# Performance work log

Measured on AMD Instinct MI355X. Metric: run time of the kernel, lower is better.

Reference implementation:

```python
import jax, jax.numpy as jnp
import numpy as np
import math

D_MODEL = 2048
NUM_HEADS = 16
D_K = D_MODEL // NUM_HEADS  # 128
SEQ_LEN = 2048
THETA = 10000.0
BATCH = 2


def setup_inputs() -> dict:
    key = jax.random.key(0)
    ks = jax.random.split(key, 5)
    std = (2.0 / (D_MODEL + D_MODEL)) ** 0.5
    return {
        "x": jax.random.normal(ks[0], (BATCH, SEQ_LEN, D_MODEL), dtype=jnp.float32),
        "Wq": jax.random.normal(ks[1], (D_MODEL, D_MODEL), dtype=jnp.float32) * std,
        "Wk": jax.random.normal(ks[2], (D_MODEL, D_MODEL), dtype=jnp.float32) * std,
        "Wv": jax.random.normal(ks[3], (D_MODEL, D_MODEL), dtype=jnp.float32) * std,
        "Wo": jax.random.normal(ks[4], (D_MODEL, D_MODEL), dtype=jnp.float32) * std,
    }


def _rope(t):
    # t: [B, H, S, d_k]; apply rotary embedding on interleaved even/odd pairs
    S = t.shape[-2]
    dk = t.shape[-1]
    inv_freq = jnp.exp(-math.log(THETA) * jnp.arange(0, dk, 2, dtype=jnp.float32) / dk)  # [dk/2]
    pos = jnp.arange(S, dtype=jnp.float32)
    freqs = pos[:, None] * inv_freq[None, :]  # [S, dk/2]
    cos = jnp.cos(freqs)
    sin = jnp.sin(freqs)
    t1 = t[..., ::2]   # [B, H, S, dk/2]
    t2 = t[..., 1::2]
    rot = jnp.stack([t1 * cos - t2 * sin, t1 * sin + t2 * cos], axis=-1)  # [B,H,S,dk/2,2]
    return rot.reshape(t.shape)


def reference(x, Wq, Wk, Wv, Wo):
    B, S, D = x.shape
    H, dk = NUM_HEADS, D // NUM_HEADS

    def split_heads(t):
        return t.reshape(B, S, H, dk).transpose(0, 2, 1, 3)  # [B,H,S,dk]

    q = split_heads(x @ Wq.T)
    k = split_heads(x @ Wk.T)
    v = split_heads(x @ Wv.T)

    q = _rope(q)
    k = _rope(k)

    scores = jnp.einsum("bhqd,bhkd->bhqk", q, k) / math.sqrt(dk)  # [B,H,S,S]
    causal = jnp.tril(jnp.ones((S, S), dtype=bool))
    scores = jnp.where(causal[None, None], scores, -jnp.inf)
    attn = jax.nn.softmax(scores, axis=-1)
    ctx = jnp.einsum("bhqk,bhkd->bhqd", attn, v)  # [B,H,S,dk]
    ctx = ctx.transpose(0, 2, 1, 3).reshape(B, S, D)
    return ctx @ Wo.T
```

## Files before the change

### kernel.cpp

```cpp
#include <hip/hip_runtime.h>
#include <stdint.h>
#include <type_traits>

#define S_LEN 2048
#define DM 2048
#define NH 16
#define DKH 128
#define NB 2
#define NROWS (NB * S_LEN)

typedef unsigned short u16;
typedef __attribute__((ext_vector_type(8))) __bf16 bf16x8;
typedef __attribute__((ext_vector_type(4))) float f32x4;

__device__ __forceinline__ float bf2f(u16 u) {
  union { unsigned u; float f; } v; v.u = ((unsigned)u) << 16; return v.f;
}
__device__ __forceinline__ u16 f2bf(float f) {
  union { float f; unsigned u; } v; v.f = f;
  unsigned r = v.u + 0x7FFFu + ((v.u >> 16) & 1u);
  return (u16)(r >> 16);
}

__device__ __forceinline__ void async_copy16(void* lds, const void* g) {
  __builtin_amdgcn_global_load_lds(
      (const __attribute__((address_space(1))) unsigned int*)g,
      (__attribute__((address_space(3))) unsigned int*)lds, 16, 0, 0);
}

__global__ void cast_all_kernel(const float* __restrict__ x, const float* __restrict__ wq,
                                const float* __restrict__ wk, const float* __restrict__ wv,
                                const float* __restrict__ wo, u16* __restrict__ xb,
                                u16* __restrict__ wqkv, u16* __restrict__ wob) {
  const int XN4 = NROWS * DM / 4;
  const int WN4 = DM * DM / 4;
  int total = XN4 + 4 * WN4;
  int stride = gridDim.x * blockDim.x;
  for (int i = blockIdx.x * blockDim.x + threadIdx.x; i < total; i += stride) {
    const float* s;
    u16* d;
    int j;
    if (i < XN4) {
      s = x; d = xb; j = i;
    } else {
      int k = i - XN4;
      int w = k >> 20;
      j = k & 0xFFFFF;
      if (w == 0) { s = wq; d = wqkv; }
      else if (w == 1) { s = wk; d = wqkv + (size_t)DM * DM; }
      else if (w == 2) { s = wv; d = wqkv + (size_t)2 * DM * DM; }
      else { s = wo; d = wob; }
    }
    float4 v = ((const float4*)s)[j];
    unsigned r0 = (unsigned)f2bf(v.x) | ((unsigned)f2bf(v.y) << 16);
    unsigned r1 = (unsigned)f2bf(v.z) | ((unsigned)f2bf(v.w) << 16);
    ((uint2*)d)[j] = make_uint2(r0, r1);
  }
}

__global__ void rope_table_kernel(float2* __restrict__ ctab) {
  int idx = blockIdx.x * blockDim.x + threadIdx.x;
  if (idx >= S_LEN * 64) return;
  int s = idx >> 6, i = idx & 63;
  float inv = expf(-9.210340371976184f * (float)i * (1.0f / 64.0f));
  float fr = (float)s * inv;
  ctab[idx] = make_float2(cosf(fr), sinf(fr));
}

template <int NSEG, int EPI>
__global__ __launch_bounds__(512, 1) void gemm256_kernel(const u16* __restrict__ A,
                                                         const u16* __restrict__ B,
                                                         void* __restrict__ C0,
                                                         void* __restrict__ C1,
                                                         void* __restrict__ C2,
                                                         const float2* __restrict__ ctab,
                                                         int M, int N, int Kd) {
  constexpr int BN = 64 * NSEG;
  constexpr int BSZ = BN * 128;
  constexpr int LDS_AE = 0, LDS_AO = 32768, LDS_BE = 65536, LDS_BO = 65536 + BSZ;

  extern __shared__ char smem[];
  u16* lds = (u16*)smem;

  int tid = threadIdx.x;
  int lane = tid & 63, wave = tid >> 6;
  int lr = lane & 15, lg = lane >> 4;
  int wm = wave >> 2, wn = wave & 3;

  int gx = gridDim.x, nwg = gx * gridDim.y;
  int bid = blockIdx.y * gx + blockIdx.x;
  int cpx = nwg >> 3;
  int swz = (bid & 7) * cpx + (bid >> 3);
  int tm = (swz / gx) * 256, tn = (swz % gx) * BN;

  int srow_in = lane >> 3;
  int scolb = ((lane & 7) * 16) ^ ((lane >> 3) << 4);

  const u16* Arows = A + (size_t)tm * Kd;
  const u16* Brows = B + (size_t)tn * Kd;

  auto stageA = [&](int aBase, int h, int kt) {
#pragma unroll
    for (int l = 0; l < 2; l++) {
      int ch = h * 16 + l * 8 + wave;
      async_copy16(lds + ((aBase + ch * 1024) >> 1),
                   Arows + (size_t)(ch * 8 + srow_in) * Kd + kt * 64 + (scolb >> 1));
    }
  };
  auto stageB = [&](int bBase, int s, int kt) {
    int ch = s * 8 + wave;
    async_copy16(lds + ((bBase + ch * 1024) >> 1),
                 Brows + (size_t)(ch * 8 + srow_in) * Kd + kt * 64 + (scolb >> 1));
  };

  int acolb[2];
#pragma unroll
  for (int ks = 0; ks < 2; ks++) acolb[ks] = (ks * 64 + lg * 16) ^ ((lr & 7) << 4);
  int aBaseW = wm * 128 * 128;
  int brow_b = (wn * 16 * NSEG + lr) * 128;

  f32x4 zero4 = {0.f, 0.f, 0.f, 0.f};
  f32x4 acc[8][NSEG];
#pragma unroll
  for (int i = 0; i < 8; i++)
#pragma unroll
    for (int j = 0; j < NSEG; j++) acc[i][j] = zero4;

  bf16x8 bpre[NSEG][2];
  bf16x8 af[2][2];

  auto loadB = [&](int bBase) {
#pragma unroll
    for (int nf = 0; nf < NSEG; nf++)
#pragma unroll
      for (int ks = 0; ks < 2; ks++)
        bpre[nf][ks] = *(const bf16x8*)&lds[(bBase + brow_b + nf * 2048 + acolb[ks]) >> 1];
  };
  auto readA = [&](int aBase, int q) {
#pragma unroll
    for (int dm = 0; dm < 2; dm++)
#pragma unroll
      for (int ks = 0; ks < 2; ks++)
        af[dm][ks] = *(const bf16x8*)&lds[(aBase + aBaseW + (2 * q + dm) * 2048 + lr * 128 +
                                           acolb[ks]) >> 1];
  };
  auto mfmaC = [&](auto qc) {
    constexpr int Q = decltype(qc)::value;
    __builtin_amdgcn_s_setprio(1);
#pragma unroll
    for (int dm = 0; dm < 2; dm++)
#pragma unroll
      for (int nf = 0; nf < NSEG; nf++)
#pragma unroll
        for (int ks = 0; ks < 2; ks++)
          acc[2 * Q + dm][nf] = __builtin_amdgcn_mfma_f32_16x16x32_bf16(
              af[dm][ks], bpre[nf][ks], acc[2 * Q + dm][nf], 0, 0, 0);
    __builtin_amdgcn_s_setprio(0);
  };
  auto bar_pre = [&]() {
    __builtin_amdgcn_s_barrier();
    asm volatile("s_waitcnt lgkmcnt(0)" ::: "memory");
    __builtin_amdgcn_sched_barrier(0);
  };
  auto vm_wait = [&]() {
    if constexpr (NSEG == 3) asm volatile("s_waitcnt vmcnt(3)" ::: "memory");
    else asm volatile("s_waitcnt vmcnt(2)" ::: "memory");
  };

  int nk = Kd >> 6;
  int nIter = nk >> 1;

  stageA(LDS_AE, 0, 0);
  stageA(LDS_AE, 1, 0);
#pragma unroll
  for (int s = 0; s < NSEG; s++) stageB(LDS_BE, s, 0);
#pragma unroll
  for (int s = 0; s < NSEG; s++) stageB(LDS_BO, s, 1);
  vm_wait();
  __builtin_amdgcn_s_barrier();

  for (int i = 0; i < nIter; i++) {
    int tO = 2 * i + 1;
    int tE2 = 2 * i + 2; if (tE2 > nk - 1) tE2 = nk - 1;
    int tO2 = 2 * i + 3; if (tO2 > nk - 1) tO2 = nk - 1;

    loadB(LDS_BE); readA(LDS_AE, 0);
    stageA(LDS_AO, 0, tO);
    asm volatile("s_waitcnt lgkmcnt(8)" ::: "memory");
    bar_pre();
    mfmaC(std::integral_constant<int, 0>{});
    __builtin_amdgcn_s_barrier();
    readA(LDS_AE, 1);
    stageA(LDS_AO, 1, tO);
    bar_pre();
    mfmaC(std::integral_constant<int, 1>{});
    __builtin_amdgcn_s_barrier();
    readA(LDS_AE, 2);
    stageB(LDS_BE, 0, tE2);
    if constexpr (NSEG == 3) stageB(LDS_BE, 1, tE2);
    bar_pre();
    mfmaC(std::integral_constant<int, 2>{});
    __builtin_amdgcn_s_barrier();
    readA(LDS_AE, 3);
    stageB(LDS_BE, NSEG - 1, tE2);
    vm_wait();
    bar_pre();
    mfmaC(std::integral_constant<int, 3>{});
    __builtin_amdgcn_s_barrier();
    loadB(LDS_BO); readA(LDS_AO, 0);
    stageA(LDS_AE, 0, tE2);
    asm volatile("s_waitcnt lgkmcnt(8)" ::: "memory");
    bar_pre();
    mfmaC(std::integral_constant<int, 0>{});
    __builtin_amdgcn_s_barrier();
    readA(LDS_AO, 1);
    stageA(LDS_AE, 1, tE2);
    bar_pre();
    mfmaC(std::integral_constant<int, 1>{});
    __builtin_amdgcn_s_barrier();
    readA(LDS_AO, 2);
    stageB(LDS_BO, 0, tO2);
    if constexpr (NSEG == 3) stageB(LDS_BO, 1, tO2);
    bar_pre();
    mfmaC(std::integral_constant<int, 2>{});
    __builtin_amdgcn_s_barrier();
    readA(LDS_AO, 3);
    stageB(LDS_BO, NSEG - 1, tO2);
    vm_wait();
    bar_pre();
    mfmaC(std::integral_constant<int, 3>{});
    __builtin_amdgcn_s_barrier();
  }

  asm volatile("s_waitcnt vmcnt(0)" ::: "memory");

#pragma unroll
  for (int mf = 0; mf < 8; mf++) {
    int row = tm + wm * 128 + mf * 16 + lg * 4;
#pragma unroll
    for (int nf = 0; nf < NSEG; nf++) {
      int col = tn + wn * 16 * NSEG + nf * 16 + lr;
      if constexpr (EPI == 0) {
        float* O = (float*)C0;
#pragma unroll
        for (int r = 0; r < 4; r++) O[(size_t)(row + r) * N + col] = acc[mf][nf][r];
      } else {
        int mat = col >> 11, lc = col & 2047;
        if (mat < 2) {
          u16* O = (mat == 0) ? (u16*)C0 : (u16*)C1;
          int d = lc & 127;
          bool odd = (d & 1) != 0;
          const float2* ct = ctab + (d >> 1);
#pragma unroll
          for (int r = 0; r < 4; r++) {
            float a = acc[mf][nf][r];
            float p = __shfl_xor(a, 1);
            int sIdx = (row + r) & (S_LEN - 1);
            float2 cs = ct[sIdx * 64];
            float o = odd ? (p * cs.y + a * cs.x) : (a * cs.x - p * cs.y);
            O[(size_t)(row + r) * 2048 + lc] = f2bf(o);
          }
        } else {
          u16* O = (u16*)C2;
          int h = lc >> 7, d = lc & 127;
          int bb = row >> 11, s0 = row & 2047;
          unsigned w0 = (unsigned)f2bf(acc[mf][nf][0]) | ((unsigned)f2bf(acc[mf][nf][1]) << 16);
          unsigned w1 = (unsigned)f2bf(acc[mf][nf][2]) | ((unsigned)f2bf(acc[mf][nf][3]) << 16);
          *(uint2*)(O + ((size_t)((bb * 16 + h) * 128 + d) * 2048 + s0)) = make_uint2(w0, w1);
        }
      }
    }
  }
}

__device__ __forceinline__ int kidx(int row, int colb) {
  return ((row << 8) + (colb ^ ((row & 7) << 4))) >> 1;
}
__device__ __forceinline__ int vidx(int row, int colb) {
  return ((row << 7) + (colb ^ ((row & 7) << 4))) >> 1;
}

__global__ __launch_bounds__(256, 2) void attn_kernel(const u16* __restrict__ Q,
                                                      const u16* __restrict__ K,
                                                      const u16* __restrict__ Vt,
                                                      u16* __restrict__ ctx) {
  __shared__ u16 Kl[2][64 * 128];
  __shared__ u16 Vl[2][128 * 64];

  int tid = threadIdx.x;
  int lane = tid & 63, wave = tid >> 6;
  int lr = lane & 15, lg = lane >> 4;
  int bh = blockIdx.x;
  int b = bh >> 4, h = bh & 15;
  int qt = (gridDim.y - 1) - blockIdx.y;
  int q0 = qt * 128;
  int q0w = q0 + wave * 32;

  bf16x8 qf[2][4];
#pragma unroll
  for (int mf = 0; mf < 2; mf++) {
    const u16* qbase = Q + (size_t)(b * S_LEN + q0w + mf * 16 + lr) * DM + h * DKH;
#pragma unroll
    for (int ks = 0; ks < 4; ks++) qf[mf][ks] = *(const bf16x8*)(qbase + ks * 32 + lg * 8);
  }

  f32x4 zero4 = {0.f, 0.f, 0.f, 0.f};
  f32x4 acc[2][8];
#pragma unroll
  for (int mf = 0; mf < 2; mf++)
#pragma unroll
    for (int f = 0; f < 8; f++) acc[mf][f] = zero4;
  float m_r[2], l_r[2];
#pragma unroll
  for (int mf = 0; mf < 2; mf++) { m_r[mf] = -3.0e38f; l_r[mf] = 0.f; }

  const float SL2E = 1.4426950408889634f * 0.08838834764831845f;
  const float RTHR = 64.0f;

  const u16* Kbh = K + (size_t)b * S_LEN * DM + h * DKH;
  const u16* Vbh = Vt + (size_t)(b * NH + h) * DKH * S_LEN;

  auto stage = [&](int buf, int kv0s) {
#pragma unroll
    for (int c = 0; c < 4; c++) {
      int ch = wave * 4 + c;
      int krow = ch * 4 + (lane >> 4);
      int kphi = (krow & 0x23) | ((krow & 0x10) >> 2) | ((krow & 0x0C) << 1);
      int kcb = ((((lane & 15) << 4) ^ ((krow & 7) << 4)) >> 1);
      async_copy16(&Kl[buf][ch * 512], Kbh + (size_t)(kv0s + kphi) * DM + kcb);
      int vrow = ch * 8 + (lane >> 3);
      int vcb = ((((lane & 7) << 4) ^ ((vrow & 7) << 4)) >> 1);
      async_copy16(&Vl[buf][ch * 512], Vbh + (size_t)vrow * S_LEN + kv0s + vcb);
    }
  };

  int ntiles = 2 * qt + 2;
  stage(0, 0);
  __syncthreads();
  int cur = 0;

  for (int t = 0; t < ntiles; t++) {
    int kv0 = t * 64;
    if (t + 1 < ntiles) stage(cur ^ 1, (t + 1) * 64);

    if (kv0 <= q0w + 31) {
      bool need_mask = (kv0 + 63 > q0w);

      f32x4 sf[4][2];
#pragma unroll
      for (int kf = 0; kf < 4; kf++)
#pragma unroll
        for (int mf = 0; mf < 2; mf++) sf[kf][mf] = zero4;
      __builtin_amdgcn_s_setprio(1);
#pragma unroll
      for (int ks = 0; ks < 4; ks++)
#pragma unroll
        for (int kf = 0; kf < 4; kf++) {
          bf16x8 kfrag = *(const bf16x8*)&Kl[cur][kidx(kf * 16 + lr, ks * 64 + lg * 16)];
          sf[kf][0] = __builtin_amdgcn_mfma_f32_16x16x32_bf16(kfrag, qf[0][ks], sf[kf][0], 0, 0, 0);
          sf[kf][1] = __builtin_amdgcn_mfma_f32_16x16x32_bf16(kfrag, qf[1][ks], sf[kf][1], 0, 0, 0);
        }
      __builtin_amdgcn_s_setprio(0);

      float sv[2][4][4];
      float mx[2];
#pragma unroll
      for (int mf = 0; mf < 2; mf++) {
        int qg = q0w + mf * 16 + lr;
        mx[mf] = -3.0e38f;
#pragma unroll
        for (int kf = 0; kf < 4; kf++) {
          int kvb = kv0 + (kf >> 1) * 32 + (kf & 1) * 4 + lg * 8;
#pragma unroll
          for (int r = 0; r < 4; r++) {
            float x = sf[kf][mf][r];
            if (need_mask) x = (kvb + r <= qg) ? x : -3.0e38f;
            sv[mf][kf][r] = x;
            mx[mf] = fmaxf(mx[mf], x);
          }
        }
        mx[mf] = fmaxf(mx[mf], __shfl_xor(mx[mf], 16));
        mx[mf] = fmaxf(mx[mf], __shfl_xor(mx[mf], 32));
      }

      bool need = (mx[0] > m_r[0] + RTHR) | (mx[1] > m_r[1] + RTHR);
      if (__any(need)) {
        float scs[2];
#pragma unroll
        for (int mf = 0; mf < 2; mf++) {
          float mnew = fmaxf(m_r[mf], mx[mf]);
          scs[mf] = __builtin_amdgcn_exp2f((m_r[mf] - mnew) * SL2E);
          m_r[mf] = mnew;
          l_r[mf] *= scs[mf];
        }
#pragma unroll
        for (int mf = 0; mf < 2; mf++) {
#pragma unroll
          for (int r = 0; r < 4; r++) {
            float sa = __shfl(scs[mf], (lane & 0x30) | (lg * 4 + r));
#pragma unroll
            for (int f = 0; f < 8; f++) acc[mf][f][r] *= sa;
          }
        }
      }

      bf16x8 pf[2][2];
#pragma unroll
      for (int mf = 0; mf < 2; mf++) {
        float rs = 0.f;
#pragma unroll
        for (int kf = 0; kf < 4; kf++)
#pragma unroll
          for (int r = 0; r < 4; r++) {
            float p = __builtin_amdgcn_exp2f((sv[mf][kf][r] - m_r[mf]) * SL2E);
            sv[mf][kf][r] = p;
            rs += p;
          }
        rs += __shfl_xor(rs, 16);
        rs += __shfl_xor(rs, 32);
        l_r[mf] += rs;
#pragma unroll
        for (int ks2 = 0; ks2 < 2; ks2++) {
          bf16x8 t2;
#pragma unroll
          for (int r = 0; r < 4; r++) {
            t2[r] = (__bf16)sv[mf][2 * ks2][r];
            t2[4 + r] = (__bf16)sv[mf][2 * ks2 + 1][r];
          }
          pf[mf][ks2] = t2;
        }
      }

      __builtin_amdgcn_s_setprio(1);
#pragma unroll
      for (int ks2 = 0; ks2 < 2; ks2++)
#pragma unroll
        for (int f = 0; f < 8; f++) {
          bf16x8 vf = *(const bf16x8*)&Vl[cur][vidx(f * 16 + lr, ks2 * 64 + lg * 16)];
          acc[0][f] = __builtin_amdgcn_mfma_f32_16x16x32_bf16(pf[0][ks2], vf, acc[0][f], 0, 0, 0);
          acc[1][f] = __builtin_amdgcn_mfma_f32_16x16x32_bf16(pf[1][ks2], vf, acc[1][f], 0, 0, 0);
        }
      __builtin_amdgcn_s_setprio(0);
    }
    __syncthreads();
    cur ^= 1;
  }

#pragma unroll
  for (int mf = 0; mf < 2; mf++) {
    float invl = 1.0f / l_r[mf];
#pragma unroll
    for (int r = 0; r < 4; r++) {
      float ia = __shfl(invl, (lane & 0x30) | (lg * 4 + r));
      int rowg = b * S_LEN + q0w + mf * 16 + lg * 4 + r;
#pragma unroll
      for (int f = 0; f < 8; f++) {
        int colg = h * DKH + f * 16 + lr;
        ctx[(size_t)rowg * DM + colg] = f2bf(acc[mf][f][r] * ia);
      }
    }
  }
}

extern "C" void kernel_launch(void* const* d_in, const int* in_sizes, int n_in,
                              void* d_out, int out_size, void* d_ws, size_t ws_size,
                              hipStream_t stream) {
  const float* x = (const float*)d_in[0];
  const float* Wq = (const float*)d_in[1];
  const float* Wk = (const float*)d_in[2];
  const float* Wv = (const float*)d_in[3];
  const float* Wo = (const float*)d_in[4];
  float* out = (float*)d_out;

  char* ws = (char*)d_ws;
  size_t off = 0;
  auto alloc = [&](size_t bytes) -> char* {
    char* p = ws + off;
    off += (bytes + 255) & ~(size_t)255;
    return p;
  };
  u16* xb = (u16*)alloc((size_t)NROWS * DM * 2);
  u16* wqkv = (u16*)alloc((size_t)3 * DM * DM * 2);
  u16* wob = (u16*)alloc((size_t)DM * DM * 2);
  u16* Qb = (u16*)alloc((size_t)NROWS * DM * 2);
  u16* Kb = (u16*)alloc((size_t)NROWS * DM * 2);
  u16* Vtb = (u16*)alloc((size_t)NROWS * DM * 2);
  float2* ctab = (float2*)alloc((size_t)S_LEN * 64 * 8);
  u16* ctx = xb;

  hipFuncSetAttribute((const void*)gemm256_kernel<3, 2>,
                      hipFuncAttributeMaxDynamicSharedMemorySize, 65536 + 2 * 192 * 128);
  hipFuncSetAttribute((const void*)gemm256_kernel<2, 0>,
                      hipFuncAttributeMaxDynamicSharedMemorySize, 65536 + 2 * 128 * 128);

  cast_all_kernel<<<2048, 256, 0, stream>>>(x, Wq, Wk, Wv, Wo, xb, wqkv, wob);
  rope_table_kernel<<<(S_LEN * 64 + 255) / 256, 256, 0, stream>>>(ctab);

  gemm256_kernel<3, 2><<<dim3(3 * DM / 192, NROWS / 256), 512, 65536 + 2 * 192 * 128, stream>>>(
      xb, wqkv, Qb, Kb, Vtb, ctab, NROWS, 3 * DM, DM);

  attn_kernel<<<dim3(NB * NH, S_LEN / 128), 256, 0, stream>>>(Qb, Kb, Vtb, ctx);

  gemm256_kernel<2, 0><<<dim3(DM / 128, NROWS / 256), 512, 65536 + 2 * 128 * 128, stream>>>(
      ctx, wob, out, nullptr, nullptr, nullptr, NROWS, DM, DM);
}
```

Before: 251.8 us.

## Replace two-stage unrolled GEMM pipeline with triple-buffered A and fixed 128-wide tiles

Rewrites the GEMM main loop from an unrolled even/odd double-buffer scheme into a per-k-tile loop. A goes through three rotating LDS buffers and B through two toggled buffers, with prefetch distance two. The QKV projection drops its 192-wide N tile for a 128-wide one, which adds workgroups and shrinks per-workgroup reuse. LDS use rises to 128 KiB, and prefetching deeper is meant to hide global-load latency behind MFMA work.

```diff
diff --git a/kernel.cpp b/kernel.cpp
--- a/kernel.cpp
+++ b/kernel.cpp
@@ -67,18 +67,20 @@
   ctab[idx] = make_float2(cosf(fr), sinf(fr));
 }
 
-template <int NSEG, int EPI>
-__global__ __launch_bounds__(512, 1) void gemm256_kernel(const u16* __restrict__ A,
+#define A_BUF0 0
+#define A_BUF1 32768
+#define A_BUF2 65536
+#define B_BUF0 98304
+#define B_TOGGLE 16384
+
+template <int EPI>
+__global__ __launch_bounds__(512, 1) void gemm4ph_kernel(const u16* __restrict__ A,
                                                          const u16* __restrict__ B,
                                                          void* __restrict__ C0,
                                                          void* __restrict__ C1,
                                                          void* __restrict__ C2,
                                                          const float2* __restrict__ ctab,
                                                          int M, int N, int Kd) {
-  constexpr int BN = 64 * NSEG;
-  constexpr int BSZ = BN * 128;
-  constexpr int LDS_AE = 0, LDS_AO = 32768, LDS_BE = 65536, LDS_BO = 65536 + BSZ;
-
   extern __shared__ char smem[];
   u16* lds = (u16*)smem;
 
@@ -91,7 +93,7 @@
   int bid = blockIdx.y * gx + blockIdx.x;
   int cpx = nwg >> 3;
   int swz = (bid & 7) * cpx + (bid >> 3);
-  int tm = (swz / gx) * 256, tn = (swz % gx) * BN;
+  int tm = (swz / gx) * 256, tn = (swz % gx) * 128;
 
   int srow_in = lane >> 3;
   int scolb = ((lane & 7) * 16) ^ ((lane >> 3) << 4);
@@ -116,22 +118,22 @@
   int acolb[2];
 #pragma unroll
   for (int ks = 0; ks < 2; ks++) acolb[ks] = (ks * 64 + lg * 16) ^ ((lr & 7) << 4);
-  int aBaseW = wm * 128 * 128;
-  int brow_b = (wn * 16 * NSEG + lr) * 128;
+  int aBaseW = wm * 16384;
+  int brow_b = (wn * 32 + lr) * 128;
 
   f32x4 zero4 = {0.f, 0.f, 0.f, 0.f};
-  f32x4 acc[8][NSEG];
+  f32x4 acc[8][2];
 #pragma unroll
   for (int i = 0; i < 8; i++)
 #pragma unroll
-    for (int j = 0; j < NSEG; j++) acc[i][j] = zero4;
-
-  bf16x8 bpre[NSEG][2];
+    for (int j = 0; j < 2; j++) acc[i][j] = zero4;
+
+  bf16x8 bpre[2][2];
   bf16x8 af[2][2];
 
   auto loadB = [&](int bBase) {
 #pragma unroll
-    for (int nf = 0; nf < NSEG; nf++)
+    for (int nf = 0; nf < 2; nf++)
 #pragma unroll
       for (int ks = 0; ks < 2; ks++)
         bpre[nf][ks] = *(const bf16x8*)&lds[(bBase + brow_b + nf * 2048 + acolb[ks]) >> 1];
@@ -150,7 +152,7 @@
 #pragma unroll
     for (int dm = 0; dm < 2; dm++)
 #pragma unroll
-      for (int nf = 0; nf < NSEG; nf++)
+      for (int nf = 0; nf < 2; nf++)
 #pragma unroll
         for (int ks = 0; ks < 2; ks++)
           acc[2 * Q + dm][nf] = __builtin_amdgcn_mfma_f32_16x16x32_bf16(
@@ -162,74 +164,48 @@
     asm volatile("s_waitcnt lgkmcnt(0)" ::: "memory");
     __builtin_amdgcn_sched_barrier(0);
   };
-  auto vm_wait = [&]() {
-    if constexpr (NSEG == 3) asm volatile("s_waitcnt vmcnt(3)" ::: "memory");
-    else asm volatile("s_waitcnt vmcnt(2)" ::: "memory");
-  };
 
   int nk = Kd >> 6;
-  int nIter = nk >> 1;
-
-  stageA(LDS_AE, 0, 0);
-  stageA(LDS_AE, 1, 0);
-#pragma unroll
-  for (int s = 0; s < NSEG; s++) stageB(LDS_BE, s, 0);
-#pragma unroll
-  for (int s = 0; s < NSEG; s++) stageB(LDS_BO, s, 1);
-  vm_wait();
+
+  int aCur = A_BUF0, aNext = A_BUF1, aN2 = A_BUF2;
+  int bCur = B_BUF0;
+
+  stageA(A_BUF0, 0, 0);
+  stageA(A_BUF0, 1, 0);
+  stageB(B_BUF0, 0, 0);
+  stageB(B_BUF0, 1, 0);
+  stageA(A_BUF1, 0, 1);
+  stageA(A_BUF1, 1, 1);
+  stageB(B_BUF0 ^ B_TOGGLE, 0, 1);
+  stageB(B_BUF0 ^ B_TOGGLE, 1, 1);
+  asm volatile("s_waitcnt vmcnt(6)" ::: "memory");
   __builtin_amdgcn_s_barrier();
 
-  for (int i = 0; i < nIter; i++) {
-    int tO = 2 * i + 1;
-    int tE2 = 2 * i + 2; if (tE2 > nk - 1) tE2 = nk - 1;
-    int tO2 = 2 * i + 3; if (tO2 > nk - 1) tO2 = nk - 1;
-
-    loadB(LDS_BE); readA(LDS_AE, 0);
-    stageA(LDS_AO, 0, tO);
-    asm volatile("s_waitcnt lgkmcnt(8)" ::: "memory");
+  for (int t = 0; t < nk; t++) {
+    int kt2 = t + 2; if (kt2 > nk - 1) kt2 = nk - 1;
+    loadB(bCur); readA(aCur, 0);
+    stageA(aN2, 0, kt2);
     bar_pre();
     mfmaC(std::integral_constant<int, 0>{});
     __builtin_amdgcn_s_barrier();
-    readA(LDS_AE, 1);
-    stageA(LDS_AO, 1, tO);
+    readA(aCur, 1);
+    stageA(aN2, 1, kt2);
     bar_pre();
     mfmaC(std::integral_constant<int, 1>{});
     __builtin_amdgcn_s_barrier();
-    readA(LDS_AE, 2);
-    stageB(LDS_BE, 0, tE2);
-    if constexpr (NSEG == 3) stageB(LDS_BE, 1, tE2);
+    readA(aCur, 2);
+    stageB(bCur, 0, kt2);
     bar_pre();
     mfmaC(std::integral_constant<int, 2>{});
     __builtin_amdgcn_s_barrier();
-    readA(LDS_AE, 3);
-    stageB(LDS_BE, NSEG - 1, tE2);
-    vm_wait();
+    readA(aCur, 3);
+    stageB(bCur, 1, kt2);
+    asm volatile("s_waitcnt vmcnt(6)" ::: "memory");
     bar_pre();
     mfmaC(std::integral_constant<int, 3>{});
     __builtin_amdgcn_s_barrier();
-    loadB(LDS_BO); readA(LDS_AO, 0);
-    stageA(LDS_AE, 0, tE2);
-    asm volatile("s_waitcnt lgkmcnt(8)" ::: "memory");
-    bar_pre();
-    mfmaC(std::integral_constant<int, 0>{});
-    __builtin_amdgcn_s_barrier();
-    readA(LDS_AO, 1);
-    stageA(LDS_AE, 1, tE2);
-    bar_pre();
-    mfmaC(std::integral_constant<int, 1>{});
-    __builtin_amdgcn_s_barrier();
-    readA(LDS_AO, 2);
-    stageB(LDS_BO, 0, tO2);
-    if constexpr (NSEG == 3) stageB(LDS_BO, 1, tO2);
-    bar_pre();
-    mfmaC(std::integral_constant<int, 2>{});
-    __builtin_amdgcn_s_barrier();
-    readA(LDS_AO, 3);
-    stageB(LDS_BO, NSEG - 1, tO2);
-    vm_wait();
-    bar_pre();
-    mfmaC(std::integral_constant<int, 3>{});
-    __builtin_amdgcn_s_barrier();
+    int tmp = aCur; aCur = aNext; aNext = aN2; aN2 = tmp;
+    bCur ^= B_TOGGLE;
   }
 
   asm volatile("s_waitcnt vmcnt(0)" ::: "memory");
@@ -238,8 +214,8 @@
   for (int mf = 0; mf < 8; mf++) {
     int row = tm + wm * 128 + mf * 16 + lg * 4;
 #pragma unroll
-    for (int nf = 0; nf < NSEG; nf++) {
-      int col = tn + wn * 16 * NSEG + nf * 16 + lr;
+    for (int nf = 0; nf < 2; nf++) {
+      int col = tn + wn * 32 + nf * 16 + lr;
       if constexpr (EPI == 0) {
         float* O = (float*)C0;
 #pragma unroll
@@ -488,19 +464,19 @@
   float2* ctab = (float2*)alloc((size_t)S_LEN * 64 * 8);
   u16* ctx = xb;
 
-  hipFuncSetAttribute((const void*)gemm256_kernel<3, 2>,
-                      hipFuncAttributeMaxDynamicSharedMemorySize, 65536 + 2 * 192 * 128);
-  hipFuncSetAttribute((const void*)gemm256_kernel<2, 0>,
-                      hipFuncAttributeMaxDynamicSharedMemorySize, 65536 + 2 * 128 * 128);
+  hipFuncSetAttribute((const void*)gemm4ph_kernel<2>,
+                      hipFuncAttributeMaxDynamicSharedMemorySize, 131072);
+  hipFuncSetAttribute((const void*)gemm4ph_kernel<0>,
+                      hipFuncAttributeMaxDynamicSharedMemorySize, 131072);
 
   cast_all_kernel<<<2048, 256, 0, stream>>>(x, Wq, Wk, Wv, Wo, xb, wqkv, wob);
   rope_table_kernel<<<(S_LEN * 64 + 255) / 256, 256, 0, stream>>>(ctab);
 
-  gemm256_kernel<3, 2><<<dim3(3 * DM / 192, NROWS / 256), 512, 65536 + 2 * 192 * 128, stream>>>(
+  gemm4ph_kernel<2><<<dim3(3 * DM / 128, NROWS / 256), 512, 131072, stream>>>(
       xb, wqkv, Qb, Kb, Vtb, ctab, NROWS, 3 * DM, DM);
 
   attn_kernel<<<dim3(NB * NH, S_LEN / 128), 256, 0, stream>>>(Qb, Kb, Vtb, ctx);
 
-  gemm256_kernel<2, 0><<<dim3(DM / 128, NROWS / 256), 512, 65536 + 2 * 128 * 128, stream>>>(
+  gemm4ph_kernel<0><<<dim3(DM / 128, NROWS / 256), 512, 131072, stream>>>(
       ctx, wob, out, nullptr, nullptr, nullptr, NROWS, DM, DM);
 }
```

Result: slower. 277.4 us (+10.1%).

## Pair short and long causal query tiles per attention block for load balance

Applied to the files above, without the earlier changes.

The attention kernel now runs 512-thread blocks, each owning two 128-row query tiles, p and 15-p, so every block does a similar amount of causal work. Each wave takes 16 rows from each tile, and a templated tile-compute lambda runs both halves while the short tile is still active, then only the long one. K/V staging is split across 8 waves and shared by both tiles, which halves the grid and removes the tail imbalance of the causal triangle. The cost is one block per CU under the new launch bounds, and more waves idle on the mask-only or single-half path.

```diff
diff --git a/kernel.cpp b/kernel.cpp
--- a/kernel.cpp
+++ b/kernel.cpp
@@ -254,10 +254,10 @@
 #pragma unroll
           for (int r = 0; r < 4; r++) {
             float a = acc[mf][nf][r];
-            float p = __shfl_xor(a, 1);
+            float pp = __shfl_xor(a, 1);
             int sIdx = (row + r) & (S_LEN - 1);
             float2 cs = ct[sIdx * 64];
-            float o = odd ? (p * cs.y + a * cs.x) : (a * cs.x - p * cs.y);
+            float o = odd ? (pp * cs.y + a * cs.x) : (a * cs.x - pp * cs.y);
             O[(size_t)(row + r) * 2048 + lc] = f2bf(o);
           }
         } else {
@@ -280,7 +280,7 @@
   return ((row << 7) + (colb ^ ((row & 7) << 4))) >> 1;
 }
 
-__global__ __launch_bounds__(256, 2) void attn_kernel(const u16* __restrict__ Q,
+__global__ __launch_bounds__(512, 1) void attn_kernel(const u16* __restrict__ Q,
                                                       const u16* __restrict__ K,
                                                       const u16* __restrict__ Vt,
                                                       u16* __restrict__ ctx) {
@@ -292,14 +292,15 @@
   int lr = lane & 15, lg = lane >> 4;
   int bh = blockIdx.x;
   int b = bh >> 4, h = bh & 15;
-  int qt = (gridDim.y - 1) - blockIdx.y;
-  int q0 = qt * 128;
-  int q0w = q0 + wave * 32;
+  int p = blockIdx.y;
+  int q0s = p * 128 + wave * 16;
+  int q0b = (15 - p) * 128 + wave * 16;
 
   bf16x8 qf[2][4];
 #pragma unroll
   for (int mf = 0; mf < 2; mf++) {
-    const u16* qbase = Q + (size_t)(b * S_LEN + q0w + mf * 16 + lr) * DM + h * DKH;
+    int base = mf ? q0b : q0s;
+    const u16* qbase = Q + (size_t)(b * S_LEN + base + lr) * DM + h * DKH;
 #pragma unroll
     for (int ks = 0; ks < 4; ks++) qf[mf][ks] = *(const bf16x8*)(qbase + ks * 32 + lg * 8);
   }
@@ -322,8 +323,8 @@
 
   auto stage = [&](int buf, int kv0s) {
 #pragma unroll
-    for (int c = 0; c < 4; c++) {
-      int ch = wave * 4 + c;
+    for (int c = 0; c < 2; c++) {
+      int ch = wave * 2 + c;
       int krow = ch * 4 + (lane >> 4);
       int kphi = (krow & 0x23) | ((krow & 0x10) >> 2) | ((krow & 0x0C) << 1);
       int kcb = ((((lane & 15) << 4) ^ ((krow & 7) << 4)) >> 1);
@@ -334,125 +335,146 @@
     }
   };
 
-  int ntiles = 2 * qt + 2;
+  auto tileCompute = [&](int kv0, int bufIdx, auto nMfC) {
+    constexpr int NMF = decltype(nMfC)::value;
+    f32x4 sf[4][NMF];
+#pragma unroll
+    for (int kf = 0; kf < 4; kf++)
+#pragma unroll
+      for (int mi = 0; mi < NMF; mi++) sf[kf][mi] = zero4;
+    __builtin_amdgcn_s_setprio(1);
+#pragma unroll
+    for (int ks = 0; ks < 4; ks++)
+#pragma unroll
+      for (int kf = 0; kf < 4; kf++) {
+        bf16x8 kfrag = *(const bf16x8*)&Kl[bufIdx][kidx(kf * 16 + lr, ks * 64 + lg * 16)];
+#pragma unroll
+        for (int mi = 0; mi < NMF; mi++) {
+          int mf = (NMF == 2) ? mi : 1;
+          sf[kf][mi] = __builtin_amdgcn_mfma_f32_16x16x32_bf16(kfrag, qf[mf][ks], sf[kf][mi], 0, 0, 0);
+        }
+      }
+    __builtin_amdgcn_s_setprio(0);
+
+    float sv[NMF][4][4];
+    float mx[NMF];
+#pragma unroll
+    for (int mi = 0; mi < NMF; mi++) {
+      int mf = (NMF == 2) ? mi : 1;
+      int base = mf ? q0b : q0s;
+      int qg = base + lr;
+      bool need_mask = (kv0 + 63 > base);
+      mx[mi] = -3.0e38f;
+#pragma unroll
+      for (int kf = 0; kf < 4; kf++) {
+        int kvb = kv0 + (kf >> 1) * 32 + (kf & 1) * 4 + lg * 8;
+#pragma unroll
+        for (int r = 0; r < 4; r++) {
+          float x = sf[kf][mi][r];
+          if (need_mask) x = (kvb + r <= qg) ? x : -3.0e38f;
+          sv[mi][kf][r] = x;
+          mx[mi] = fmaxf(mx[mi], x);
+        }
+      }
+      mx[mi] = fmaxf(mx[mi], __shfl_xor(mx[mi], 16));
+      mx[mi] = fmaxf(mx[mi], __shfl_xor(mx[mi], 32));
+    }
+
+    bool need = false;
+#pragma unroll
+    for (int mi = 0; mi < NMF; mi++) {
+      int mf = (NMF == 2) ? mi : 1;
+      need = need | (mx[mi] > m_r[mf] + RTHR);
+    }
+    if (__any(need)) {
+      float scs[NMF];
+#pragma unroll
+      for (int mi = 0; mi < NMF; mi++) {
+        int mf = (NMF == 2) ? mi : 1;
+        float mnew = fmaxf(m_r[mf], mx[mi]);
+        scs[mi] = __builtin_amdgcn_exp2f((m_r[mf] - mnew) * SL2E);
+        m_r[mf] = mnew;
+        l_r[mf] *= scs[mi];
+      }
+#pragma unroll
+      for (int mi = 0; mi < NMF; mi++) {
+        int mf = (NMF == 2) ? mi : 1;
+#pragma unroll
+        for (int r = 0; r < 4; r++) {
+          float sa = __shfl(scs[mi], (lane & 0x30) | (lg * 4 + r));
+#pragma unroll
+          for (int f = 0; f < 8; f++) acc[mf][f][r] *= sa;
+        }
+      }
+    }
+
+    bf16x8 pf[NMF][2];
+#pragma unroll
+    for (int mi = 0; mi < NMF; mi++) {
+      int mf = (NMF == 2) ? mi : 1;
+      float rs = 0.f;
+#pragma unroll
+      for (int kf = 0; kf < 4; kf++)
+#pragma unroll
+        for (int r = 0; r < 4; r++) {
+          float pv = __builtin_amdgcn_exp2f((sv[mi][kf][r] - m_r[mf]) * SL2E);
+          sv[mi][kf][r] = pv;
+          rs += pv;
+        }
+      rs += __shfl_xor(rs, 16);
+      rs += __shfl_xor(rs, 32);
+      l_r[mf] += rs;
+#pragma unroll
+      for (int ks2 = 0; ks2 < 2; ks2++) {
+        bf16x8 t2;
+#pragma unroll
+        for (int r = 0; r < 4; r++) {
+          t2[r] = (__bf16)sv[mi][2 * ks2][r];
+          t2[4 + r] = (__bf16)sv[mi][2 * ks2 + 1][r];
+        }
+        pf[mi][ks2] = t2;
+      }
+    }
+
+    __builtin_amdgcn_s_setprio(1);
+#pragma unroll
+    for (int ks2 = 0; ks2 < 2; ks2++)
+#pragma unroll
+      for (int f = 0; f < 8; f++) {
+        bf16x8 vf = *(const bf16x8*)&Vl[bufIdx][vidx(f * 16 + lr, ks2 * 64 + lg * 16)];
+#pragma unroll
+        for (int mi = 0; mi < NMF; mi++) {
+          int mf = (NMF == 2) ? mi : 1;
+          acc[mf][f] = __builtin_amdgcn_mfma_f32_16x16x32_bf16(pf[mi][ks2], vf, acc[mf][f], 0, 0, 0);
+        }
+      }
+    __builtin_amdgcn_s_setprio(0);
+  };
+
+  int ntB = 2 * (15 - p) + 2;
   stage(0, 0);
   __syncthreads();
   int cur = 0;
 
-  for (int t = 0; t < ntiles; t++) {
+  for (int t = 0; t < ntB; t++) {
     int kv0 = t * 64;
-    if (t + 1 < ntiles) stage(cur ^ 1, (t + 1) * 64);
-
-    if (kv0 <= q0w + 31) {
-      bool need_mask = (kv0 + 63 > q0w);
-
-      f32x4 sf[4][2];
-#pragma unroll
-      for (int kf = 0; kf < 4; kf++)
-#pragma unroll
-        for (int mf = 0; mf < 2; mf++) sf[kf][mf] = zero4;
-      __builtin_amdgcn_s_setprio(1);
-#pragma unroll
-      for (int ks = 0; ks < 4; ks++)
-#pragma unroll
-        for (int kf = 0; kf < 4; kf++) {
-          bf16x8 kfrag = *(const bf16x8*)&Kl[cur][kidx(kf * 16 + lr, ks * 64 + lg * 16)];
-          sf[kf][0] = __builtin_amdgcn_mfma_f32_16x16x32_bf16(kfrag, qf[0][ks], sf[kf][0], 0, 0, 0);
-          sf[kf][1] = __builtin_amdgcn_mfma_f32_16x16x32_bf16(kfrag, qf[1][ks], sf[kf][1], 0, 0, 0);
-        }
-      __builtin_amdgcn_s_setprio(0);
-
-      float sv[2][4][4];
-      float mx[2];
-#pragma unroll
-      for (int mf = 0; mf < 2; mf++) {
-        int qg = q0w + mf * 16 + lr;
-        mx[mf] = -3.0e38f;
-#pragma unroll
-        for (int kf = 0; kf < 4; kf++) {
-          int kvb = kv0 + (kf >> 1) * 32 + (kf & 1) * 4 + lg * 8;
-#pragma unroll
-          for (int r = 0; r < 4; r++) {
-            float x = sf[kf][mf][r];
-            if (need_mask) x = (kvb + r <= qg) ? x : -3.0e38f;
-            sv[mf][kf][r] = x;
-            mx[mf] = fmaxf(mx[mf], x);
-          }
-        }
-        mx[mf] = fmaxf(mx[mf], __shfl_xor(mx[mf], 16));
-        mx[mf] = fmaxf(mx[mf], __shfl_xor(mx[mf], 32));
-      }
-
-      bool need = (mx[0] > m_r[0] + RTHR) | (mx[1] > m_r[1] + RTHR);
-      if (__any(need)) {
-        float scs[2];
-#pragma unroll
-        for (int mf = 0; mf < 2; mf++) {
-          float mnew = fmaxf(m_r[mf], mx[mf]);
-          scs[mf] = __builtin_amdgcn_exp2f((m_r[mf] - mnew) * SL2E);
-          m_r[mf] = mnew;
-          l_r[mf] *= scs[mf];
-        }
-#pragma unroll
-        for (int mf = 0; mf < 2; mf++) {
-#pragma unroll
-          for (int r = 0; r < 4; r++) {
-            float sa = __shfl(scs[mf], (lane & 0x30) | (lg * 4 + r));
-#pragma unroll
-            for (int f = 0; f < 8; f++) acc[mf][f][r] *= sa;
-          }
-        }
-      }
-
-      bf16x8 pf[2][2];
-#pragma unroll
-      for (int mf = 0; mf < 2; mf++) {
-        float rs = 0.f;
-#pragma unroll
-        for (int kf = 0; kf < 4; kf++)
-#pragma unroll
-          for (int r = 0; r < 4; r++) {
-            float p = __builtin_amdgcn_exp2f((sv[mf][kf][r] - m_r[mf]) * SL2E);
-            sv[mf][kf][r] = p;
-            rs += p;
-          }
-        rs += __shfl_xor(rs, 16);
-        rs += __shfl_xor(rs, 32);
-        l_r[mf] += rs;
-#pragma unroll
-        for (int ks2 = 0; ks2 < 2; ks2++) {
-          bf16x8 t2;
-#pragma unroll
-          for (int r = 0; r < 4; r++) {
-            t2[r] = (__bf16)sv[mf][2 * ks2][r];
-            t2[4 + r] = (__bf16)sv[mf][2 * ks2 + 1][r];
-          }
-          pf[mf][ks2] = t2;
-        }
-      }
-
-      __builtin_amdgcn_s_setprio(1);
-#pragma unroll
-      for (int ks2 = 0; ks2 < 2; ks2++)
-#pragma unroll
-        for (int f = 0; f < 8; f++) {
-          bf16x8 vf = *(const bf16x8*)&Vl[cur][vidx(f * 16 + lr, ks2 * 64 + lg * 16)];
-          acc[0][f] = __builtin_amdgcn_mfma_f32_16x16x32_bf16(pf[0][ks2], vf, acc[0][f], 0, 0, 0);
-          acc[1][f] = __builtin_amdgcn_mfma_f32_16x16x32_bf16(pf[1][ks2], vf, acc[1][f], 0, 0, 0);
-        }
-      __builtin_amdgcn_s_setprio(0);
-    }
+    if (t + 1 < ntB) stage(cur ^ 1, (t + 1) * 64);
+    bool actS = (kv0 <= q0s + 15);
+    bool actB = (kv0 <= q0b + 15);
+    if (actS) tileCompute(kv0, cur, std::integral_constant<int, 2>{});
+    else if (actB) tileCompute(kv0, cur, std::integral_constant<int, 1>{});
     __syncthreads();
     cur ^= 1;
   }
 
 #pragma unroll
   for (int mf = 0; mf < 2; mf++) {
+    int base = mf ? q0b : q0s;
     float invl = 1.0f / l_r[mf];
 #pragma unroll
     for (int r = 0; r < 4; r++) {
       float ia = __shfl(invl, (lane & 0x30) | (lg * 4 + r));
-      int rowg = b * S_LEN + q0w + mf * 16 + lg * 4 + r;
+      int rowg = b * S_LEN + base + lg * 4 + r;
 #pragma unroll
       for (int f = 0; f < 8; f++) {
         int colg = h * DKH + f * 16 + lr;
@@ -499,7 +521,7 @@
   gemm256_kernel<3, 2><<<dim3(3 * DM / 192, NROWS / 256), 512, 65536 + 2 * 192 * 128, stream>>>(
       xb, wqkv, Qb, Kb, Vtb, ctab, NROWS, 3 * DM, DM);
 
-  attn_kernel<<<dim3(NB * NH, S_LEN / 128), 256, 0, stream>>>(Qb, Kb, Vtb, ctx);
+  attn_kernel<<<dim3(NB * NH, 8), 512, 0, stream>>>(Qb, Kb, Vtb, ctx);
 
   gemm256_kernel<2, 0><<<dim3(DM / 128, NROWS / 256), 512, 65536 + 2 * 128 * 128, stream>>>(
       ctx, wob, out, nullptr, nullptr, nullptr, NROWS, DM, DM);
```

Result: faster. 243.5 us (-3.3%).
